# Kernel tuning notes

Measured on AMD Instinct MI355X. Metric: run time of the kernel, lower is better.

## Reference

```python
import jax, jax.numpy as jnp
import numpy as np

B, S, D = 128, 512, 1024          # batch, ctx seqlen, model dim
GEN_V, INP_V, OUT_V = 50000, 30000, 50257  # gen vocab, input vocab, output vocab


def setup_inputs() -> dict:
    key = jax.random.key(0)
    ks = jax.random.split(key, 7)
    x = jax.random.normal(ks[0], (B, D), jnp.float32)
    alphas = jax.random.uniform(ks[1], (B, S), jnp.float32)
    alphas = alphas / alphas.sum(-1, keepdims=True)  # normalized attention probs
    ctx_inp = jax.random.randint(ks[2], (B, S), 0, INP_V)
    gen_to_out = jax.random.randint(ks[3], (GEN_V,), 0, OUT_V)
    inp_to_out = jax.random.randint(ks[4], (INP_V,), 0, OUT_V)
    W_gate = jax.random.normal(ks[5], (D, 1), jnp.float32) * 0.02
    b_gate = jnp.zeros((1,), jnp.float32)
    W_gen = jax.random.normal(ks[6], (D, GEN_V), jnp.float32) * 0.02
    b_gen = jnp.zeros((GEN_V,), jnp.float32)
    return {"x": x, "alphas": alphas, "W_gate": W_gate, "b_gate": b_gate,
            "W_gen": W_gen, "b_gen": b_gen, "ctx_inp": ctx_inp,
            "gen_to_out": gen_to_out, "inp_to_out": inp_to_out}


def reference(x, alphas, W_gate, b_gate, W_gen, b_gen, ctx_inp, gen_to_out, inp_to_out):
    # gate: probability of generating vs pointing  [B,1]
    interp = jax.nn.sigmoid(x @ W_gate + b_gate)
    # generation distribution over gen vocab       [B,GEN_V]
    gen_probs = jax.nn.softmax(x @ W_gen + b_gen, axis=-1)
    # scatter_add gen probs into output vocab (same index map for all rows)
    out_gen = jax.ops.segment_sum(gen_probs.T, gen_to_out, num_segments=OUT_V).T  # [B,OUT_V]
    # scatter_add pointer probs into output vocab (per-row indices)
    ctx_out = inp_to_out[ctx_inp]  # [B,S]
    rows = jnp.arange(x.shape[0])[:, None]
    out_ptr = jnp.zeros((x.shape[0], OUT_V), x.dtype).at[rows, ctx_out].add(alphas)
    # interpolated mixture
    return interp * out_gen + (1.0 - interp) * out_ptr
```

## Files before the change

### kernel.cpp

```cpp
#include <hip/hip_runtime.h>
#include <hip/hip_bf16.h>

#define B_DIM 128
#define S_DIM 512
#define D_DIM 1024
#define GEN_VV 50000
#define OUT_VV 50257

typedef float f32x4 __attribute__((ext_vector_type(4)));
typedef __bf16 bf16x8 __attribute__((ext_vector_type(8)));
typedef __bf16 bf16x4 __attribute__((ext_vector_type(4)));
typedef __bf16 bf16x2 __attribute__((ext_vector_type(2)));

__global__ __launch_bounds__(256) void k_gate(const float* __restrict__ x,
        const float* __restrict__ Wg, const float* __restrict__ bgate,
        __bf16* __restrict__ xb, float* __restrict__ interp) {
    __shared__ float red[4];
    const int b = blockIdx.x, t = threadIdx.x;
    float4 xv = reinterpret_cast<const float4*>(x + (size_t)b * D_DIM)[t];
    float4 wv = reinterpret_cast<const float4*>(Wg)[t];
    float dot = xv.x * wv.x + xv.y * wv.y + xv.z * wv.z + xv.w * wv.w;
    bf16x4 hb;
    hb[0] = (__bf16)xv.x; hb[1] = (__bf16)xv.y; hb[2] = (__bf16)xv.z; hb[3] = (__bf16)xv.w;
    reinterpret_cast<bf16x4*>(xb + (size_t)b * D_DIM)[t] = hb;
#pragma unroll
    for (int m = 32; m >= 1; m >>= 1) dot += __shfl_xor(dot, m);
    if ((t & 63) == 0) red[t >> 6] = dot;
    __syncthreads();
    if (t == 0) {
        float d = red[0] + red[1] + red[2] + red[3] + bgate[0];
        interp[b] = 1.0f / (1.0f + __expf(-d));
    }
}

__global__ __launch_bounds__(256) void k_gemm(const __bf16* __restrict__ xb,
        const float* __restrict__ W, const float* __restrict__ bgen,
        float* __restrict__ logits) {
    __shared__ __align__(16) __bf16 As[128 * 40];
    __shared__ __align__(16) __bf16 Ws[64 * 40];
    const int t = threadIdx.x;
    const int lane = t & 63;
    const int wv = t >> 6;
    const int wrow = wv * 32;
    const int g = lane >> 4;
    const int r16 = lane & 15;
    const int nb = blockIdx.x * 64;

    const int wk = (t >> 4) * 2;
    const int wn = (t & 15) * 4;
    const bool wval = (nb + wn) < GEN_VV;

    f32x4 acc[2][4];
#pragma unroll
    for (int i = 0; i < 2; i++)
#pragma unroll
        for (int j = 0; j < 4; j++) acc[i][j] = (f32x4){0.f, 0.f, 0.f, 0.f};

    for (int k0 = 0; k0 < D_DIM; k0 += 32) {
        {
            const int r0 = t >> 2, kc0 = t & 3;
            *reinterpret_cast<uint4*>(&As[r0 * 40 + kc0 * 8]) =
                *reinterpret_cast<const uint4*>(&xb[(size_t)r0 * D_DIM + k0 + kc0 * 8]);
            const int c1 = t + 256;
            const int r1 = c1 >> 2, kc1 = c1 & 3;
            *reinterpret_cast<uint4*>(&As[r1 * 40 + kc1 * 8]) =
                *reinterpret_cast<const uint4*>(&xb[(size_t)r1 * D_DIM + k0 + kc1 * 8]);
        }
        {
            const float* p = W + (size_t)(k0 + wk) * GEN_VV + (nb + wn);
            float4 ra = wval ? *reinterpret_cast<const float4*>(p) : make_float4(0.f, 0.f, 0.f, 0.f);
            float4 rb = wval ? *reinterpret_cast<const float4*>(p + GEN_VV) : make_float4(0.f, 0.f, 0.f, 0.f);
            float fa[4] = {ra.x, ra.y, ra.z, ra.w};
            float fb[4] = {rb.x, rb.y, rb.z, rb.w};
#pragma unroll
            for (int j = 0; j < 4; j++) {
                bf16x2 pr;
                pr[0] = (__bf16)fa[j];
                pr[1] = (__bf16)fb[j];
                *reinterpret_cast<bf16x2*>(&Ws[(wn + j) * 40 + wk]) = pr;
            }
        }
        __syncthreads();
        bf16x8 af[2];
#pragma unroll
        for (int rf = 0; rf < 2; rf++) {
            bf16x4 lo = *reinterpret_cast<const bf16x4*>(&As[(wrow + rf * 16 + r16) * 40 + g * 4]);
            bf16x4 hi = *reinterpret_cast<const bf16x4*>(&As[(wrow + rf * 16 + r16) * 40 + 16 + g * 4]);
            af[rf] = __builtin_shufflevector(lo, hi, 0, 1, 2, 3, 4, 5, 6, 7);
        }
#pragma unroll
        for (int cf = 0; cf < 4; cf++) {
            bf16x4 lo = *reinterpret_cast<const bf16x4*>(&Ws[(cf * 16 + r16) * 40 + g * 4]);
            bf16x4 hi = *reinterpret_cast<const bf16x4*>(&Ws[(cf * 16 + r16) * 40 + 16 + g * 4]);
            bf16x8 bfr = __builtin_shufflevector(lo, hi, 0, 1, 2, 3, 4, 5, 6, 7);
#pragma unroll
            for (int rf = 0; rf < 2; rf++)
                acc[rf][cf] = __builtin_amdgcn_mfma_f32_16x16x32_bf16(af[rf], bfr, acc[rf][cf], 0, 0, 0);
        }
        __syncthreads();
    }
#pragma unroll
    for (int cf = 0; cf < 4; cf++) {
        const int col = nb + cf * 16 + r16;
        if (col < GEN_VV) {
            const float bg = bgen[col];
#pragma unroll
            for (int rf = 0; rf < 2; rf++) {
                const int row = wrow + rf * 16 + g * 4;
#pragma unroll
                for (int j = 0; j < 4; j++)
                    logits[(size_t)(row + j) * GEN_VV + col] = acc[rf][cf][j] + bg;
            }
        }
    }
}

__global__ __launch_bounds__(1024) void k_stats(const float* __restrict__ logits,
        float* __restrict__ stats) {
    __shared__ float red[16];
    __shared__ float bcast;
    const int b = blockIdx.x, t = threadIdx.x;
    const float4* row = reinterpret_cast<const float4*>(logits + (size_t)b * GEN_VV);
    float m = -1e30f;
    for (int i = t; i < GEN_VV / 4; i += 1024) {
        float4 v = row[i];
        m = fmaxf(m, fmaxf(fmaxf(v.x, v.y), fmaxf(v.z, v.w)));
    }
#pragma unroll
    for (int d = 32; d >= 1; d >>= 1) m = fmaxf(m, __shfl_xor(m, d));
    if ((t & 63) == 0) red[t >> 6] = m;
    __syncthreads();
    if (t == 0) {
        float M = red[0];
        for (int i = 1; i < 16; i++) M = fmaxf(M, red[i]);
        bcast = M;
    }
    __syncthreads();
    const float M = bcast;
    float s = 0.f;
    for (int i = t; i < GEN_VV / 4; i += 1024) {
        float4 v = row[i];
        s += __expf(v.x - M) + __expf(v.y - M) + __expf(v.z - M) + __expf(v.w - M);
    }
#pragma unroll
    for (int d = 32; d >= 1; d >>= 1) s += __shfl_xor(s, d);
    if ((t & 63) == 0) red[t >> 6] = s;
    __syncthreads();
    if (t == 0) {
        float S = 0.f;
        for (int i = 0; i < 16; i++) S += red[i];
        stats[2 * b] = M;
        stats[2 * b + 1] = 1.0f / S;
    }
}

__global__ __launch_bounds__(256) void k_hist(const int* __restrict__ g2o, int* __restrict__ hist) {
    int v = blockIdx.x * 256 + threadIdx.x;
    if (v < GEN_VV) atomicAdd(&hist[g2o[v]], 1);
}

__global__ __launch_bounds__(1024) void k_scan(const int* __restrict__ hist, int* __restrict__ offs) {
    __shared__ int sums[1024];
    const int t = threadIdx.x;
    const int lo = t * 50;
    const int hiS = (lo + 50 < OUT_VV) ? lo + 50 : OUT_VV;
    int s = 0;
    for (int i = lo; i < hiS; i++) s += hist[i];
    sums[t] = s;
    __syncthreads();
    for (int d = 1; d < 1024; d <<= 1) {
        int v = (t >= d) ? sums[t - d] : 0;
        __syncthreads();
        sums[t] += v;
        __syncthreads();
    }
    int run = sums[t] - s;
    const int hiW = (lo + 50 < OUT_VV + 1) ? lo + 50 : OUT_VV + 1;
    for (int i = lo; i < hiW; i++) {
        offs[i] = run;
        if (i < OUT_VV) run += hist[i];
    }
}

__global__ __launch_bounds__(256) void k_scatter(const int* __restrict__ g2o,
        const int* __restrict__ offs, int* __restrict__ cursor, int* __restrict__ items) {
    int v = blockIdx.x * 256 + threadIdx.x;
    if (v < GEN_VV) {
        int o = g2o[v];
        int slot = atomicAdd(&cursor[o], 1);
        items[offs[o] + slot] = v;
    }
}

__global__ __launch_bounds__(256) void k_prob_t(const float* __restrict__ logits,
        const float* __restrict__ stats, const float* __restrict__ interp,
        float* __restrict__ PT) {
    __shared__ float tile[32][33];
    const int v0 = blockIdx.x * 32, b0 = blockIdx.y * 32;
    const int t = threadIdx.x;
    const int tv = t & 31, p = t >> 5;
#pragma unroll
    for (int q = 0; q < 4; q++) {
        const int b = b0 + p + 8 * q;
        const int v = v0 + tv;
        float val = 0.f;
        if (v < GEN_VV) {
            const float M = stats[2 * b], is = stats[2 * b + 1];
            val = __expf(logits[(size_t)b * GEN_VV + v] - M) * is * interp[b];
        }
        tile[tv][p + 8 * q] = val;
    }
    __syncthreads();
#pragma unroll
    for (int q = 0; q < 4; q++) {
        const int v = v0 + p + 8 * q;
        const int b = b0 + tv;
        if (v < GEN_VV) PT[(size_t)v * B_DIM + b] = tile[p + 8 * q][tv];
    }
}

__global__ __launch_bounds__(256) void k_gather(const float* __restrict__ PT,
        const int* __restrict__ offs, const int* __restrict__ items,
        float* __restrict__ out) {
    __shared__ float tile[64][129];
    const int o0 = blockIdx.x * 64;
    const int t = threadIdx.x;
    const int grp = t >> 7;
    const int b = t & 127;
    for (int oi = grp; oi < 64; oi += 2) {
        const int o = o0 + oi;
        float acc = 0.f;
        if (o < OUT_VV) {
            const int base = offs[o], end = offs[o + 1];
            for (int idx = base; idx < end; idx++) {
                const int v = items[idx];
                acc += PT[(size_t)v * B_DIM + b];
            }
        }
        tile[oi][b] = acc;
    }
    __syncthreads();
    const int oj = t & 63, bb = t >> 6;
    for (int bp = 0; bp < 32; bp++) {
        const int bw = bp * 4 + bb;
        const int o = o0 + oj;
        if (o < OUT_VV) out[(size_t)bw * OUT_VV + o] = tile[oj][bw];
    }
}

__global__ __launch_bounds__(256) void k_ptr(const float* __restrict__ alphas,
        const int* __restrict__ ctx, const int* __restrict__ i2o,
        const float* __restrict__ interp, float* __restrict__ out) {
    const int i = blockIdx.x * 256 + threadIdx.x;
    const int b = i >> 9;
    const int o = i2o[ctx[i]];
    atomicAdd(&out[(size_t)b * OUT_VV + o], (1.0f - interp[b]) * alphas[i]);
}

extern "C" void kernel_launch(void* const* d_in, const int* in_sizes, int n_in,
                              void* d_out, int out_size, void* d_ws, size_t ws_size,
                              hipStream_t stream) {
    const float* x      = (const float*)d_in[0];
    const float* alphas = (const float*)d_in[1];
    const float* Wgate  = (const float*)d_in[2];
    const float* bgate  = (const float*)d_in[3];
    const float* Wgen   = (const float*)d_in[4];
    const float* bgen   = (const float*)d_in[5];
    const int*   ctx    = (const int*)d_in[6];
    const int*   g2o    = (const int*)d_in[7];
    const int*   i2o    = (const int*)d_in[8];
    float* out = (float*)d_out;

    char* w = (char*)d_ws;
    float* PT = (float*)w;          w += (size_t)GEN_VV * B_DIM * 4;
    __bf16* xb = (__bf16*)w;        w += (size_t)B_DIM * D_DIM * 2;
    float* interp = (float*)w;      w += 512;
    float* stats = (float*)w;       w += 1024;
    int* hist = (int*)w;            w += OUT_VV * 4;
    int* cursor = (int*)w;          w += OUT_VV * 4;
    int* offs = (int*)w;            w += (OUT_VV + 1) * 4;
    int* items = (int*)w;           w += GEN_VV * 4;

    float* logits = out;

    hipMemsetAsync(hist, 0, (size_t)2 * OUT_VV * sizeof(int), stream);

    k_gate<<<B_DIM, 256, 0, stream>>>(x, Wgate, bgate, xb, interp);
    k_gemm<<<(GEN_VV + 63) / 64, 256, 0, stream>>>(xb, Wgen, bgen, logits);
    k_stats<<<B_DIM, 1024, 0, stream>>>(logits, stats);
    k_hist<<<(GEN_VV + 255) / 256, 256, 0, stream>>>(g2o, hist);
    k_scan<<<1, 1024, 0, stream>>>(hist, offs);
    k_scatter<<<(GEN_VV + 255) / 256, 256, 0, stream>>>(g2o, offs, cursor, items);
    k_prob_t<<<dim3((GEN_VV + 31) / 32, B_DIM / 32), 256, 0, stream>>>(logits, stats, interp, PT);
    k_gather<<<(OUT_VV + 63) / 64, 256, 0, stream>>>(PT, offs, items, out);
    k_ptr<<<(B_DIM * S_DIM) / 256, 256, 0, stream>>>(alphas, ctx, i2o, interp, out);
}
```

Measured before the change: 475.5 us.

## Retile GEMM with K=64 prefetch, split stats, replace CSR gather with atomic scatter

The GEMM now uses K=64 steps with register prefetch of the next tile and a 2x2 warp layout with a padded, permuted LDS layout, so fragments are read with 128-bit loads. Row softmax stats are split into two half-row blocks that are merged later. The histogram/scan/scatter/transpose/gather pipeline is replaced by one kernel that computes probabilities and atomically adds them into a zeroed output. Logits move to the workspace. This removes four kernel launches and the PT round trip, but adds a full output memset and about 6.4M float atomics.

```diff
diff --git a/kernel.cpp b/kernel.cpp
--- a/kernel.cpp
+++ b/kernel.cpp
@@ -6,6 +6,7 @@
 #define D_DIM 1024
 #define GEN_VV 50000
 #define OUT_VV 50257
+#define LDK 72
 
 typedef float f32x4 __attribute__((ext_vector_type(4)));
 typedef __bf16 bf16x8 __attribute__((ext_vector_type(8)));
@@ -36,93 +37,124 @@
 __global__ __launch_bounds__(256) void k_gemm(const __bf16* __restrict__ xb,
         const float* __restrict__ W, const float* __restrict__ bgen,
         float* __restrict__ logits) {
-    __shared__ __align__(16) __bf16 As[128 * 40];
-    __shared__ __align__(16) __bf16 Ws[64 * 40];
+    __shared__ __align__(16) __bf16 As[128 * LDK];
+    __shared__ __align__(16) __bf16 Ws[64 * LDK];
     const int t = threadIdx.x;
-    const int lane = t & 63;
-    const int wv = t >> 6;
-    const int wrow = wv * 32;
-    const int g = lane >> 4;
-    const int r16 = lane & 15;
+    const int lane = t & 63, wv = t >> 6;
+    const int wr = wv >> 1, wc = wv & 1;
+    const int g = lane >> 4, r16 = lane & 15;
     const int nb = blockIdx.x * 64;
 
-    const int wk = (t >> 4) * 2;
-    const int wn = (t & 15) * 4;
-    const bool wval = (nb + wn) < GEN_VV;
-
-    f32x4 acc[2][4];
-#pragma unroll
-    for (int i = 0; i < 2; i++)
-#pragma unroll
-        for (int j = 0; j < 4; j++) acc[i][j] = (f32x4){0.f, 0.f, 0.f, 0.f};
-
-    for (int k0 = 0; k0 < D_DIM; k0 += 32) {
+    const int uk = t & 15, qn = t >> 4;
+    const int kk = uk * 2, nn = qn * 4;
+    const bool wval = (nb + nn + 3) < GEN_VV;
+    const int pos0 = ((kk & 15) >> 2) * 8 + (kk & 3) + 4 * (kk >> 4);
+    const int pos1 = 32 + pos0;
+
+    int a_row[4], a_kc[4], a_base[4];
+#pragma unroll
+    for (int i = 0; i < 4; i++) {
+        const int c = t + 256 * i;
+        const int row = c >> 3, kc = c & 7, m = kc & 3, s = kc >> 2;
+        const int q1 = (m & 1) * 16 + (m & 2) * 2;
+        a_row[i] = row; a_kc[i] = kc;
+        a_base[i] = row * LDK + s * 32 + q1;
+    }
+
+    f32x4 acc[4][2];
+#pragma unroll
+    for (int i = 0; i < 4; i++)
+#pragma unroll
+        for (int j = 0; j < 2; j++) acc[i][j] = (f32x4){0.f, 0.f, 0.f, 0.f};
+
+    uint4 apr[4];
+    float4 wa0, wb0, wa1, wb1;
+
+    auto loadA = [&](int k0) {
+#pragma unroll
+        for (int i = 0; i < 4; i++)
+            apr[i] = *reinterpret_cast<const uint4*>(&xb[(size_t)a_row[i] * D_DIM + k0 + a_kc[i] * 8]);
+    };
+    auto loadW = [&](int k0) {
+        const float4 z = make_float4(0.f, 0.f, 0.f, 0.f);
+        const float* p0 = W + (size_t)(k0 + kk) * GEN_VV + nb + nn;
+        const float* p1 = W + (size_t)(k0 + kk + 32) * GEN_VV + nb + nn;
+        wa0 = wval ? *reinterpret_cast<const float4*>(p0) : z;
+        wb0 = wval ? *reinterpret_cast<const float4*>(p0 + GEN_VV) : z;
+        wa1 = wval ? *reinterpret_cast<const float4*>(p1) : z;
+        wb1 = wval ? *reinterpret_cast<const float4*>(p1 + GEN_VV) : z;
+    };
+
+    loadA(0); loadW(0);
+
+    for (int step = 0; step < 16; ++step) {
+#pragma unroll
+        for (int i = 0; i < 4; i++) {
+            union { uint4 u; bf16x8 v; } cv; cv.u = apr[i];
+            *reinterpret_cast<bf16x4*>(&As[a_base[i]]) =
+                __builtin_shufflevector(cv.v, cv.v, 0, 1, 2, 3);
+            *reinterpret_cast<bf16x4*>(&As[a_base[i] + 8]) =
+                __builtin_shufflevector(cv.v, cv.v, 4, 5, 6, 7);
+        }
         {
-            const int r0 = t >> 2, kc0 = t & 3;
-            *reinterpret_cast<uint4*>(&As[r0 * 40 + kc0 * 8]) =
-                *reinterpret_cast<const uint4*>(&xb[(size_t)r0 * D_DIM + k0 + kc0 * 8]);
-            const int c1 = t + 256;
-            const int r1 = c1 >> 2, kc1 = c1 & 3;
-            *reinterpret_cast<uint4*>(&As[r1 * 40 + kc1 * 8]) =
-                *reinterpret_cast<const uint4*>(&xb[(size_t)r1 * D_DIM + k0 + kc1 * 8]);
-        }
-        {
-            const float* p = W + (size_t)(k0 + wk) * GEN_VV + (nb + wn);
-            float4 ra = wval ? *reinterpret_cast<const float4*>(p) : make_float4(0.f, 0.f, 0.f, 0.f);
-            float4 rb = wval ? *reinterpret_cast<const float4*>(p + GEN_VV) : make_float4(0.f, 0.f, 0.f, 0.f);
-            float fa[4] = {ra.x, ra.y, ra.z, ra.w};
-            float fb[4] = {rb.x, rb.y, rb.z, rb.w};
+            const float f0[4] = {wa0.x, wa0.y, wa0.z, wa0.w};
+            const float g0[4] = {wb0.x, wb0.y, wb0.z, wb0.w};
+            const float f1[4] = {wa1.x, wa1.y, wa1.z, wa1.w};
+            const float g1[4] = {wb1.x, wb1.y, wb1.z, wb1.w};
 #pragma unroll
             for (int j = 0; j < 4; j++) {
-                bf16x2 pr;
-                pr[0] = (__bf16)fa[j];
-                pr[1] = (__bf16)fb[j];
-                *reinterpret_cast<bf16x2*>(&Ws[(wn + j) * 40 + wk]) = pr;
+                bf16x2 p; p[0] = (__bf16)f0[j]; p[1] = (__bf16)g0[j];
+                *reinterpret_cast<bf16x2*>(&Ws[(nn + j) * LDK + pos0]) = p;
+                bf16x2 q; q[0] = (__bf16)f1[j]; q[1] = (__bf16)g1[j];
+                *reinterpret_cast<bf16x2*>(&Ws[(nn + j) * LDK + pos1]) = q;
             }
         }
         __syncthreads();
-        bf16x8 af[2];
-#pragma unroll
-        for (int rf = 0; rf < 2; rf++) {
-            bf16x4 lo = *reinterpret_cast<const bf16x4*>(&As[(wrow + rf * 16 + r16) * 40 + g * 4]);
-            bf16x4 hi = *reinterpret_cast<const bf16x4*>(&As[(wrow + rf * 16 + r16) * 40 + 16 + g * 4]);
-            af[rf] = __builtin_shufflevector(lo, hi, 0, 1, 2, 3, 4, 5, 6, 7);
-        }
-#pragma unroll
-        for (int cf = 0; cf < 4; cf++) {
-            bf16x4 lo = *reinterpret_cast<const bf16x4*>(&Ws[(cf * 16 + r16) * 40 + g * 4]);
-            bf16x4 hi = *reinterpret_cast<const bf16x4*>(&Ws[(cf * 16 + r16) * 40 + 16 + g * 4]);
-            bf16x8 bfr = __builtin_shufflevector(lo, hi, 0, 1, 2, 3, 4, 5, 6, 7);
-#pragma unroll
-            for (int rf = 0; rf < 2; rf++)
-                acc[rf][cf] = __builtin_amdgcn_mfma_f32_16x16x32_bf16(af[rf], bfr, acc[rf][cf], 0, 0, 0);
+        if (step < 15) { loadA((step + 1) * 64); loadW((step + 1) * 64); }
+#pragma unroll
+        for (int s = 0; s < 2; s++) {
+            bf16x8 af[4], bfr[2];
+#pragma unroll
+            for (int fr = 0; fr < 4; fr++)
+                af[fr] = *reinterpret_cast<const bf16x8*>(
+                    &As[(wr * 64 + fr * 16 + r16) * LDK + s * 32 + g * 8]);
+#pragma unroll
+            for (int fc = 0; fc < 2; fc++)
+                bfr[fc] = *reinterpret_cast<const bf16x8*>(
+                    &Ws[(wc * 32 + fc * 16 + r16) * LDK + s * 32 + g * 8]);
+#pragma unroll
+            for (int fr = 0; fr < 4; fr++)
+#pragma unroll
+                for (int fc = 0; fc < 2; fc++)
+                    acc[fr][fc] = __builtin_amdgcn_mfma_f32_16x16x32_bf16(af[fr], bfr[fc], acc[fr][fc], 0, 0, 0);
         }
         __syncthreads();
     }
-#pragma unroll
-    for (int cf = 0; cf < 4; cf++) {
-        const int col = nb + cf * 16 + r16;
+
+#pragma unroll
+    for (int fc = 0; fc < 2; fc++) {
+        const int col = nb + wc * 32 + fc * 16 + r16;
         if (col < GEN_VV) {
             const float bg = bgen[col];
 #pragma unroll
-            for (int rf = 0; rf < 2; rf++) {
-                const int row = wrow + rf * 16 + g * 4;
+            for (int fr = 0; fr < 4; fr++) {
+                const int row0 = wr * 64 + fr * 16 + g * 4;
 #pragma unroll
                 for (int j = 0; j < 4; j++)
-                    logits[(size_t)(row + j) * GEN_VV + col] = acc[rf][cf][j] + bg;
+                    logits[(size_t)(row0 + j) * GEN_VV + col] = acc[fr][fc][j] + bg;
             }
         }
     }
 }
 
-__global__ __launch_bounds__(1024) void k_stats(const float* __restrict__ logits,
-        float* __restrict__ stats) {
-    __shared__ float red[16];
-    __shared__ float bcast;
-    const int b = blockIdx.x, t = threadIdx.x;
-    const float4* row = reinterpret_cast<const float4*>(logits + (size_t)b * GEN_VV);
+__global__ __launch_bounds__(256) void k_stats(const float* __restrict__ logits,
+        float2* __restrict__ stats2) {
+    __shared__ float red[4];
+    __shared__ float bc;
+    const int bi = blockIdx.x, b = bi >> 1, h = bi & 1, t = threadIdx.x;
+    const float4* row = reinterpret_cast<const float4*>(logits + (size_t)b * GEN_VV) + h * 6250;
     float m = -1e30f;
-    for (int i = t; i < GEN_VV / 4; i += 1024) {
+    for (int i = t; i < 6250; i += 256) {
         float4 v = row[i];
         m = fmaxf(m, fmaxf(fmaxf(v.x, v.y), fmaxf(v.z, v.w)));
     }
@@ -130,15 +162,11 @@
     for (int d = 32; d >= 1; d >>= 1) m = fmaxf(m, __shfl_xor(m, d));
     if ((t & 63) == 0) red[t >> 6] = m;
     __syncthreads();
-    if (t == 0) {
-        float M = red[0];
-        for (int i = 1; i < 16; i++) M = fmaxf(M, red[i]);
-        bcast = M;
-    }
-    __syncthreads();
-    const float M = bcast;
+    if (t == 0) bc = fmaxf(fmaxf(red[0], red[1]), fmaxf(red[2], red[3]));
+    __syncthreads();
+    const float M = bc;
     float s = 0.f;
-    for (int i = t; i < GEN_VV / 4; i += 1024) {
+    for (int i = t; i < 6250; i += 256) {
         float4 v = row[i];
         s += __expf(v.x - M) + __expf(v.y - M) + __expf(v.z - M) + __expf(v.w - M);
     }
@@ -146,105 +174,37 @@
     for (int d = 32; d >= 1; d >>= 1) s += __shfl_xor(s, d);
     if ((t & 63) == 0) red[t >> 6] = s;
     __syncthreads();
-    if (t == 0) {
-        float S = 0.f;
-        for (int i = 0; i < 16; i++) S += red[i];
-        stats[2 * b] = M;
-        stats[2 * b + 1] = 1.0f / S;
-    }
-}
-
-__global__ __launch_bounds__(256) void k_hist(const int* __restrict__ g2o, int* __restrict__ hist) {
-    int v = blockIdx.x * 256 + threadIdx.x;
-    if (v < GEN_VV) atomicAdd(&hist[g2o[v]], 1);
-}
-
-__global__ __launch_bounds__(1024) void k_scan(const int* __restrict__ hist, int* __restrict__ offs) {
-    __shared__ int sums[1024];
-    const int t = threadIdx.x;
-    const int lo = t * 50;
-    const int hiS = (lo + 50 < OUT_VV) ? lo + 50 : OUT_VV;
-    int s = 0;
-    for (int i = lo; i < hiS; i++) s += hist[i];
-    sums[t] = s;
-    __syncthreads();
-    for (int d = 1; d < 1024; d <<= 1) {
-        int v = (t >= d) ? sums[t - d] : 0;
-        __syncthreads();
-        sums[t] += v;
-        __syncthreads();
-    }
-    int run = sums[t] - s;
-    const int hiW = (lo + 50 < OUT_VV + 1) ? lo + 50 : OUT_VV + 1;
-    for (int i = lo; i < hiW; i++) {
-        offs[i] = run;
-        if (i < OUT_VV) run += hist[i];
-    }
-}
-
-__global__ __launch_bounds__(256) void k_scatter(const int* __restrict__ g2o,
-        const int* __restrict__ offs, int* __restrict__ cursor, int* __restrict__ items) {
-    int v = blockIdx.x * 256 + threadIdx.x;
-    if (v < GEN_VV) {
-        int o = g2o[v];
-        int slot = atomicAdd(&cursor[o], 1);
-        items[offs[o] + slot] = v;
-    }
-}
-
-__global__ __launch_bounds__(256) void k_prob_t(const float* __restrict__ logits,
-        const float* __restrict__ stats, const float* __restrict__ interp,
-        float* __restrict__ PT) {
+    if (t == 0) stats2[bi] = make_float2(M, red[0] + red[1] + red[2] + red[3]);
+}
+
+__global__ __launch_bounds__(256) void k_probs_scatter(const float* __restrict__ logits,
+        const float2* __restrict__ stats2, const float* __restrict__ interp,
+        const int* __restrict__ g2o, float* __restrict__ out) {
     __shared__ float tile[32][33];
     const int v0 = blockIdx.x * 32, b0 = blockIdx.y * 32;
-    const int t = threadIdx.x;
-    const int tv = t & 31, p = t >> 5;
+    const int t = threadIdx.x, tv = t & 31, p = t >> 5;
 #pragma unroll
     for (int q = 0; q < 4; q++) {
         const int b = b0 + p + 8 * q;
+        const float2 s0 = stats2[2 * b], s1 = stats2[2 * b + 1];
+        const float M = fmaxf(s0.x, s1.x);
+        const float denom = s0.y * __expf(s0.x - M) + s1.y * __expf(s1.x - M);
+        const float sc = interp[b] / denom;
         const int v = v0 + tv;
         float val = 0.f;
-        if (v < GEN_VV) {
-            const float M = stats[2 * b], is = stats[2 * b + 1];
-            val = __expf(logits[(size_t)b * GEN_VV + v] - M) * is * interp[b];
-        }
+        if (v < GEN_VV) val = __expf(logits[(size_t)b * GEN_VV + v] - M) * sc;
         tile[tv][p + 8 * q] = val;
     }
     __syncthreads();
-#pragma unroll
-    for (int q = 0; q < 4; q++) {
-        const int v = v0 + p + 8 * q;
-        const int b = b0 + tv;
-        if (v < GEN_VV) PT[(size_t)v * B_DIM + b] = tile[p + 8 * q][tv];
-    }
-}
-
-__global__ __launch_bounds__(256) void k_gather(const float* __restrict__ PT,
-        const int* __restrict__ offs, const int* __restrict__ items,
-        float* __restrict__ out) {
-    __shared__ float tile[64][129];
-    const int o0 = blockIdx.x * 64;
-    const int t = threadIdx.x;
-    const int grp = t >> 7;
-    const int b = t & 127;
-    for (int oi = grp; oi < 64; oi += 2) {
-        const int o = o0 + oi;
-        float acc = 0.f;
-        if (o < OUT_VV) {
-            const int base = offs[o], end = offs[o + 1];
-            for (int idx = base; idx < end; idx++) {
-                const int v = items[idx];
-                acc += PT[(size_t)v * B_DIM + b];
-            }
-        }
-        tile[oi][b] = acc;
-    }
-    __syncthreads();
-    const int oj = t & 63, bb = t >> 6;
-    for (int bp = 0; bp < 32; bp++) {
-        const int bw = bp * 4 + bb;
-        const int o = o0 + oj;
-        if (o < OUT_VV) out[(size_t)bw * OUT_VV + o] = tile[oj][bw];
+    const int vi = t >> 3, bj = t & 7;
+    const int v = v0 + vi;
+    if (v < GEN_VV) {
+        const int o = g2o[v];
+#pragma unroll
+        for (int j = 0; j < 4; j++) {
+            const int b = b0 + bj * 4 + j;
+            atomicAdd(&out[(size_t)b * OUT_VV + o], tile[vi][bj * 4 + j]);
+        }
     }
 }
 
@@ -272,26 +232,17 @@
     float* out = (float*)d_out;
 
     char* w = (char*)d_ws;
-    float* PT = (float*)w;          w += (size_t)GEN_VV * B_DIM * 4;
+    float* logits = (float*)w;      w += (size_t)B_DIM * GEN_VV * 4;
     __bf16* xb = (__bf16*)w;        w += (size_t)B_DIM * D_DIM * 2;
     float* interp = (float*)w;      w += 512;
-    float* stats = (float*)w;       w += 1024;
-    int* hist = (int*)w;            w += OUT_VV * 4;
-    int* cursor = (int*)w;          w += OUT_VV * 4;
-    int* offs = (int*)w;            w += (OUT_VV + 1) * 4;
-    int* items = (int*)w;           w += GEN_VV * 4;
-
-    float* logits = out;
-
-    hipMemsetAsync(hist, 0, (size_t)2 * OUT_VV * sizeof(int), stream);
+    float2* stats2 = (float2*)w;    w += 2048;
+
+    hipMemsetAsync(d_out, 0, (size_t)B_DIM * OUT_VV * sizeof(float), stream);
 
     k_gate<<<B_DIM, 256, 0, stream>>>(x, Wgate, bgate, xb, interp);
     k_gemm<<<(GEN_VV + 63) / 64, 256, 0, stream>>>(xb, Wgen, bgen, logits);
-    k_stats<<<B_DIM, 1024, 0, stream>>>(logits, stats);
-    k_hist<<<(GEN_VV + 255) / 256, 256, 0, stream>>>(g2o, hist);
-    k_scan<<<1, 1024, 0, stream>>>(hist, offs);
-    k_scatter<<<(GEN_VV + 255) / 256, 256, 0, stream>>>(g2o, offs, cursor, items);
-    k_prob_t<<<dim3((GEN_VV + 31) / 32, B_DIM / 32), 256, 0, stream>>>(logits, stats, interp, PT);
-    k_gather<<<(OUT_VV + 63) / 64, 256, 0, stream>>>(PT, offs, items, out);
+    k_stats<<<2 * B_DIM, 256, 0, stream>>>(logits, stats2);
+    k_probs_scatter<<<dim3((GEN_VV + 31) / 32, B_DIM / 32), 256, 0, stream>>>(
+        logits, stats2, interp, g2o, out);
     k_ptr<<<(B_DIM * S_DIM) / 256, 256, 0, stream>>>(alphas, ctx, i2o, interp, out);
 }
```

After: 698.3 us. +46.9%, slower.
